# Kernel tuning notes

Hardware: AMD Instinct MI355X
Metric: run time of the kernel (lower is better)

## Reference

```python
import jax, jax.numpy as jnp
import numpy as np

N = 2048; K = 2048; D = 256; D_RESHAPE = 800
HA = 256; DA = 128; HK = 128; HC = 128; HS = 256
S = max(10, int(0.1 * K))  # n_sample = 204
BN_SCALE = 1.0 / float(np.sqrt(1.0 + 1e-5))  # eval BatchNorm1d with running stats (0,1)

def leaky(x):
    return jax.nn.leaky_relu(x, 0.01)

def conv2d(x, w, b):
    y = jax.lax.conv_general_dilated(x, w, (1, 1), 'VALID', dimension_numbers=('NCHW', 'OIHW', 'NCHW'))
    return y + b[None, :, None, None]

def maxpool2(x):
    return jax.lax.reduce_window(x, -jnp.inf, jax.lax.max, (1, 1, 2, 2), (1, 1, 2, 2), 'VALID')

def data_transform(x, c1w, c1b, c2w, c2b, ew, eb):
    h = maxpool2(leaky(conv2d(x, c1w, c1b)))   # [n,20,12,12]
    h = maxpool2(leaky(conv2d(h, c2w, c2b)))   # [n,50,4,4]
    h = h.reshape(-1, D_RESHAPE)
    return leaky(h @ ew.T + eb)                # [n,D]

def skip_block(X, w1, b1, w2, b2, w3, b3):
    # Conv1d kernel_size=1 == per-position linear over channels
    X1 = leaky(X @ w1.T + b1) * BN_SCALE       # [n,HC]
    X2 = leaky(X @ w2.T + b2) * BN_SCALE       # [n,HC]
    X3 = leaky(X @ w3.T + b3) * BN_SCALE       # [n,d]
    feat = jax.nn.softmax(X1 @ X2.T, axis=0)   # torch Softmax(dim=1) on [1,n,n] -> axis 0
    return feat @ X3 + X

def mask_scores(A, w1, b1, w2, b2, w3, b3, w4, b4):
    X1 = leaky(A @ w1.T + b1)                  # [n,HK]
    X2 = jnp.tanh(A @ w2.T + b2)               # [n,HK]
    M = X1.T @ X2                              # [HK,HK]
    A3 = leaky(M @ w3.T + b3)                  # [HK,K]
    s = A3.T @ w4[0] + b4[0]                   # [K]
    return jax.nn.softmax(s)

def attention(X, few, feb, vw, vb, uw, ub, aww, awb, ew, eb):
    H = leaky(X @ few.T + feb)                 # [n,HA]
    AV = jnp.tanh(H @ vw.T + vb)
    AU = leaky(H @ uw.T + ub)
    a = leaky((AV * AU) @ aww.T + awb)         # [n,1]
    A = jax.nn.softmax(a.T, axis=1)            # [1,n]
    M = leaky((A @ H) @ ew.T + eb)             # [1,d]
    return M, A

def euclid(X, Y):
    d2 = jnp.sum(X * X, 1)[:, None] + jnp.sum(Y * Y, 1)[None, :] - 2.0 * (X @ Y.T)
    return jnp.sqrt(jnp.maximum(d2, 0.0))


def setup_inputs() -> dict:
    key = jax.random.key(0)
    ks = iter(jax.random.split(key, 70))
    def rn(shape, scale=0.05):
        return jax.random.normal(next(ks), shape, dtype=jnp.float32) * scale
    d = {}
    d['B'] = jax.random.normal(next(ks), (N, 1, 28, 28), dtype=jnp.float32)
    d['KB'] = jax.random.normal(next(ks), (K, 1, 28, 28), dtype=jnp.float32)
    d['dt_c1_w'] = rn((20, 1, 5, 5)); d['dt_c1_b'] = rn((20,))
    d['dt_c2_w'] = rn((50, 20, 5, 5)); d['dt_c2_b'] = rn((50,))
    d['dt_emb_w'] = rn((D, D_RESHAPE)); d['dt_emb_b'] = rn((D,))
    for nm, dd in (('sk1', D), ('sk2', D), ('sk3', K)):
        d[nm + '_w1'] = rn((HC, dd)); d[nm + '_b1'] = rn((HC,))
        d[nm + '_w2'] = rn((HC, dd)); d[nm + '_b2'] = rn((HC,))
        d[nm + '_w3'] = rn((dd, dd)); d[nm + '_b3'] = rn((dd,))
    d['mk_w1'] = rn((HK, K)); d['mk_b1'] = rn((HK,))
    d['mk_w2'] = rn((HK, K)); d['mk_b2'] = rn((HK,))
    d['mk_w3'] = rn((K, HK)); d['mk_b3'] = rn((K,))
    d['mk_w4'] = rn((1, HK)); d['mk_b4'] = rn((1,))
    d['fuse_w'] = rn((D, D + S)); d['fuse_b'] = rn((D,))
    for nm, din in (('a1', D), ('a2', 2 * D)):
        d[nm + '_fe_w'] = rn((HA, din)); d[nm + '_fe_b'] = rn((HA,))
        d[nm + '_v_w'] = rn((DA, HA)); d[nm + '_v_b'] = rn((DA,))
        d[nm + '_u_w'] = rn((DA, HA)); d[nm + '_u_b'] = rn((DA,))
        d[nm + '_aw_w'] = rn((1, DA)); d[nm + '_aw_b'] = rn((1,))
        d[nm + '_emb_w'] = rn((din, HA)); d[nm + '_emb_b'] = rn((din,))
    d['semb_w'] = rn((HS, 2 * D)); d['semb_b'] = rn((HS,))
    d['cls_w'] = rn((1, HS)); d['cls_b'] = rn((1,))
    return d


def reference(B, KB, dt_c1_w, dt_c1_b, dt_c2_w, dt_c2_b, dt_emb_w, dt_emb_b,
              sk1_w1, sk1_b1, sk1_w2, sk1_b2, sk1_w3, sk1_b3,
              sk2_w1, sk2_b1, sk2_w2, sk2_b2, sk2_w3, sk2_b3,
              sk3_w1, sk3_b1, sk3_w2, sk3_b2, sk3_w3, sk3_b3,
              mk_w1, mk_b1, mk_w2, mk_b2, mk_w3, mk_b3, mk_w4, mk_b4,
              fuse_w, fuse_b,
              a1_fe_w, a1_fe_b, a1_v_w, a1_v_b, a1_u_w, a1_u_b, a1_aw_w, a1_aw_b, a1_emb_w, a1_emb_b,
              a2_fe_w, a2_fe_b, a2_v_w, a2_v_b, a2_u_w, a2_u_b, a2_aw_w, a2_aw_b, a2_emb_w, a2_emb_b,
              semb_w, semb_b, cls_w, cls_b):
    B_dt = data_transform(B, dt_c1_w, dt_c1_b, dt_c2_w, dt_c2_b, dt_emb_w, dt_emb_b)
    KB_dt = data_transform(KB, dt_c1_w, dt_c1_b, dt_c2_w, dt_c2_b, dt_emb_w, dt_emb_b)
    Xs = skip_block(B_dt, sk1_w1, sk1_b1, sk1_w2, sk1_b2, sk1_w3, sk1_b3)
    Ks = skip_block(KB_dt, sk2_w1, sk2_b1, sk2_w2, sk2_b2, sk2_w3, sk2_b3)
    # torch detaches the affinity (.detach().numpy())
    aff = euclid(jax.lax.stop_gradient(Xs), jax.lax.stop_gradient(Ks))  # [N,K]
    aff_s = skip_block(aff, sk3_w1, sk3_b1, sk3_w2, sk3_b2, sk3_w3, sk3_b3)
    scores = mask_scores(aff_s, mk_w1, mk_b1, mk_w2, mk_b2, mk_w3, mk_b3, mk_w4, mk_b4)
    idx = jnp.argsort(-scores)[:S]                       # top-S knowledge columns
    B_bag = jax.nn.softmax(aff_s[:, idx], axis=1)        # [N,S], torch Softmax(dim=2)
    B_fuse = leaky(jnp.concatenate([B_dt, B_bag], axis=1) @ fuse_w.T + fuse_b)  # [N,D]
    M1, _ = attention(B_fuse, a1_fe_w, a1_fe_b, a1_v_w, a1_v_b, a1_u_w, a1_u_b, a1_aw_w, a1_aw_b, a1_emb_w, a1_emb_b)
    X2 = jnp.concatenate([B_fuse, jnp.tile(M1, (B_fuse.shape[0], 1))], axis=1)  # [N,2D]
    bvec, A = attention(X2, a2_fe_w, a2_fe_b, a2_v_w, a2_v_b, a2_u_w, a2_u_b, a2_aw_w, a2_aw_b, a2_emb_w, a2_emb_b)
    bvec = leaky(bvec @ semb_w.T + semb_b)               # [1,HS]
    Y = jnp.clip(jax.nn.sigmoid(bvec @ cls_w.T + cls_b), 1e-5, 1.0 - 1e-5)
    return (Y, A)
```

## Files before the change

kernel.cpp:

```cpp
#include <hip/hip_runtime.h>
#include <math.h>

#define LEAKY(x) ((x) > 0.f ? (x) : 0.01f * (x))
static constexpr float BN_SCALE = 0.9999950000374997f;

typedef unsigned short ushort_t;
typedef float f32x4 __attribute__((ext_vector_type(4)));
typedef short bf16x8 __attribute__((ext_vector_type(8)));

__device__ __forceinline__ ushort_t f2bfu(float f) {
  union { float f; unsigned u; } v; v.f = f;
  unsigned r = v.u + 0x7fffu + ((v.u >> 16) & 1u);
  return (ushort_t)(r >> 16);
}
__device__ __forceinline__ float bfu2f(ushort_t u) {
  union { unsigned u; float f; } v; v.u = ((unsigned)u) << 16;
  return v.f;
}

__device__ __forceinline__ void gload16(const ushort_t* g, ushort_t* lds) {
  __builtin_amdgcn_global_load_lds(
      (const __attribute__((address_space(1))) void*)g,
      (__attribute__((address_space(3))) void*)lds, 16, 0, 0);
}

__global__ void fill_out(float* out, int n) {
  int i = blockIdx.x * 256 + threadIdx.x;
  if (i < n) out[i] = 0.25f;
}

struct CvtArgs {
  const float* src[20];
  ushort_t* dst[20];
  int cum[21];
};
__global__ void to_bf16_flat(CvtArgs a) {
  int total = a.cum[20];
  for (int i = blockIdx.x * 256 + threadIdx.x; i < total; i += gridDim.x * 256) {
    int s = 0;
    while (i >= a.cum[s + 1]) ++s;
    int off = i - a.cum[s];
    a.dst[s][off] = f2bfu(a.src[s][off]);
  }
}

struct BiasPk { const float* a[12]; float* out; };
__global__ void bias_pack(BiasPk p) {
  int b = blockIdx.x, t = threadIdx.x;
  p.out[b * 256 + t] = (t < 128) ? p.a[2 * b][t] : p.a[2 * b + 1][t - 128];
}

__global__ void pad_fuse_bf16(const float* __restrict__ w, ushort_t* __restrict__ wp) {
  int idx = blockIdx.x * 256 + threadIdx.x;
  if (idx >= 256 * 512) return;
  int o = idx >> 9, k = idx & 511;
  wp[idx] = (k < 460) ? f2bfu(w[(size_t)o * 460 + k]) : (ushort_t)0;
}

__global__ void w2_relayout(const float* __restrict__ w2, ushort_t* __restrict__ w2p) {
  int idx = blockIdx.x * 256 + threadIdx.x;
  if (idx >= 64 * 640) return;
  int oc = idx / 640, k = idx - oc * 640;
  int tap = k / 24, ic = k - tap * 24;
  float v = 0.f;
  if (oc < 50 && tap < 25 && ic < 20)
    v = w2[(size_t)(oc * 20 + ic) * 25 + tap];
  w2p[idx] = f2bfu(v);
}

__launch_bounds__(256)
__global__ void conv12_mfma(const float* __restrict__ imgB, const float* __restrict__ imgK,
                            const float* __restrict__ w1, const float* __restrict__ b1,
                            const ushort_t* __restrict__ w2p, const float* __restrict__ b2,
                            ushort_t* __restrict__ out800) {
  __shared__ __align__(16) char smem[41472];
  ushort_t* h1T = (ushort_t*)smem;
  ushort_t* As  = (ushort_t*)(smem + 13824);
  ushort_t* Bs  = (ushort_t*)(smem + 32256);
  float* simg = (float*)(smem + 13824);
  float* sw1  = (float*)(smem + 20992);
  float* b1s  = (float*)(smem + 23040);
  float* Cf   = (float*)smem;

  int tid = threadIdx.x;
  int bx = blockIdx.x;
  const float* imgb = (bx < 1024) ? imgB + (size_t)bx * 2 * 784
                                  : imgK + (size_t)(bx - 1024) * 2 * 784;

  for (int i = tid; i < 1568; i += 256) {
    int im = (i >= 784) ? 1 : 0;
    int r = i - im * 784;
    int row = r / 28, col = r - row * 28;
    int sc = (col + (row >> 1)) & 31;
    simg[im * 896 + row * 32 + sc] = imgb[i];
  }
  for (int i = tid; i < 500; i += 256) sw1[i] = w1[i];
  if (tid < 20) b1s[tid] = b1[tid];
  for (int i = tid; i < 288; i += 256) {
    uint2 z; z.x = 0; z.y = 0;
    *(uint2*)&h1T[i * 24 + 20] = z;
  }
  __syncthreads();

  for (int o = tid; o < 1152; o += 256) {
    int im = (o >= 576) ? 1 : 0;
    int rem = o - im * 576;
    int cg = rem / 144;
    int pos = rem - cg * 144;
    int py = pos / 12, px = pos - py * 12;
    int y0 = py * 2, x0 = px * 2;
    float p[6][6];
    #pragma unroll
    for (int yy = 0; yy < 6; ++yy) {
      int rr = y0 + yy;
      int rbase = im * 896 + rr * 32;
      int rot = rr >> 1;
      #pragma unroll
      for (int xx = 0; xx < 6; ++xx)
        p[yy][xx] = simg[rbase + ((x0 + xx + rot) & 31)];
    }
    #pragma unroll
    for (int cc = 0; cc < 5; ++cc) {
      int c = cg * 5 + cc;
      const float* wc = &sw1[c * 25];
      float bb = b1s[c];
      float t0 = bb, t1 = bb, t2 = bb, t3 = bb;
      #pragma unroll
      for (int ky = 0; ky < 5; ++ky)
        #pragma unroll
        for (int kx = 0; kx < 5; ++kx) {
          float wv = wc[ky * 5 + kx];
          t0 += p[ky][kx] * wv;
          t1 += p[ky][kx + 1] * wv;
          t2 += p[ky + 1][kx] * wv;
          t3 += p[ky + 1][kx + 1] * wv;
        }
      float mx = fmaxf(fmaxf(t0, t1), fmaxf(t2, t3));
      h1T[(im * 144 + pos) * 24 + c] = f2bfu(LEAKY(mx));
    }
  }

  int wave = tid >> 6, lane = tid & 63;
  int wm = (wave >> 1) * 64, wn = (wave & 1) * 32;
  int mrow = lane & 15, kq = lane >> 4;

  int sA_r = tid >> 1;
  int sA_j0 = (tid & 1) * 4;
  int sA_im = sA_r >> 6;
  int sA_op = sA_r & 63;
  int sA_oy = sA_op >> 3, sA_ox = sA_op & 7;
  int sB_r = tid >> 2;
  int sB_j0 = (tid & 3) * 2;

  f32x4 acc[4][2];
  #pragma unroll
  for (int i = 0; i < 4; ++i)
    #pragma unroll
    for (int j = 0; j < 2; ++j)
      #pragma unroll
      for (int r = 0; r < 4; ++r) acc[i][j][r] = 0.f;

  bf16x8 wreg[2];
  #pragma unroll
  for (int i = 0; i < 2; ++i)
    wreg[i] = *(const bf16x8*)&w2p[(size_t)sB_r * 640 + (sB_j0 + i) * 8];

  for (int kb = 0; kb < 10; ++kb) {
    __syncthreads();
    #pragma unroll
    for (int i = 0; i < 2; ++i)
      *(bf16x8*)&Bs[sB_r * 72 + (sB_j0 + i) * 8] = wreg[i];
    #pragma unroll
    for (int i = 0; i < 4; ++i) {
      int j = sA_j0 + i;
      int g = kb * 8 + j;
      int tap = g / 3;
      int part = g - tap * 3;
      bf16x8 v = {0, 0, 0, 0, 0, 0, 0, 0};
      if (tap < 25) {
        int ky = tap / 5, kx = tap - ky * 5;
        int pos = (sA_oy + ky) * 12 + sA_ox + kx;
        v = *(const bf16x8*)&h1T[(sA_im * 144 + pos) * 24 + part * 8];
      }
      *(bf16x8*)&As[sA_r * 72 + j * 8] = v;
    }
    if (kb + 1 < 10) {
      #pragma unroll
      for (int i = 0; i < 2; ++i)
        wreg[i] = *(const bf16x8*)&w2p[(size_t)sB_r * 640 + (kb + 1) * 64 + (sB_j0 + i) * 8];
    }
    __syncthreads();
    #pragma unroll
    for (int ks = 0; ks < 2; ++ks) {
      bf16x8 af[4], bf[2];
      #pragma unroll
      for (int mt = 0; mt < 4; ++mt)
        af[mt] = *(const bf16x8*)&As[(wm + mt * 16 + mrow) * 72 + ks * 32 + kq * 8];
      #pragma unroll
      for (int nt = 0; nt < 2; ++nt)
        bf[nt] = *(const bf16x8*)&Bs[(wn + nt * 16 + mrow) * 72 + ks * 32 + kq * 8];
      #pragma unroll
      for (int mt = 0; mt < 4; ++mt)
        #pragma unroll
        for (int nt = 0; nt < 2; ++nt)
          acc[mt][nt] = __builtin_amdgcn_mfma_f32_16x16x32_bf16(af[mt], bf[nt], acc[mt][nt], 0, 0, 0);
    }
  }
  __syncthreads();
  #pragma unroll
  for (int mt = 0; mt < 4; ++mt)
    #pragma unroll
    for (int nt = 0; nt < 2; ++nt) {
      int n0 = wn + nt * 16 + (lane & 15);
      #pragma unroll
      for (int r = 0; r < 4; ++r)
        Cf[(wm + mt * 16 + kq * 4 + r) * 68 + n0] = acc[mt][nt][r];
    }
  __syncthreads();
  for (int o = tid; o < 1600; o += 256) {
    int im = o / 800, oi = o - im * 800;
    int oc = oi >> 4, p = oi & 15, py = p >> 2, px = p & 3;
    int r0 = im * 64 + py * 16 + px * 2;
    float bb = b2[oc];
    float t0 = LEAKY(Cf[r0 * 68 + oc] + bb);
    float t1 = LEAKY(Cf[(r0 + 1) * 68 + oc] + bb);
    float t2 = LEAKY(Cf[(r0 + 8) * 68 + oc] + bb);
    float t3 = LEAKY(Cf[(r0 + 9) * 68 + oc] + bb);
    out800[(size_t)(bx * 2 + im) * 800 + oi] = f2bfu(fmaxf(fmaxf(t0, t1), fmaxf(t2, t3)));
  }
}

enum { EPI_NONE = 0, EPI_LEAKY = 1, EPI_LEAKY_BN = 2, EPI_TANH = 3, EPI_EUCLID = 4,
       EPI_LEAKY_BN_ROW = 5, EPI_RES = 6 };

template <int EPI>
__launch_bounds__(256)
__global__ void gemm_bf16_nt(const ushort_t* __restrict__ A, const ushort_t* __restrict__ B,
                             const float* __restrict__ bias, float* __restrict__ C32,
                             ushort_t* __restrict__ C16, int M, int N, int Kd,
                             const float* __restrict__ e1, const float* __restrict__ e2) {
  __shared__ __align__(16) ushort_t As[2][128 * 32];
  __shared__ __align__(16) ushort_t Bs[2][128 * 32];
  int tid = threadIdx.x;
  int bm = blockIdx.y * 128, bn = blockIdx.x * 128;
  int wave = tid >> 6, lane = tid & 63;
  int wm = (wave >> 1) * 64, wn = (wave & 1) * 64;
  int mrow = lane & 15, kq = lane >> 4;
  int l0 = tid, l1 = tid + 256;
  const ushort_t* ga0 = A + (size_t)(bm + (l0 >> 2)) * Kd + (l0 & 3) * 8;
  const ushort_t* ga1 = A + (size_t)(bm + (l1 >> 2)) * Kd + (l1 & 3) * 8;
  const ushort_t* gb0 = B + (size_t)(bn + (l0 >> 2)) * Kd + (l0 & 3) * 8;
  const ushort_t* gb1 = B + (size_t)(bn + (l1 >> 2)) * Kd + (l1 & 3) * 8;

  f32x4 acc[4][4];
  #pragma unroll
  for (int i = 0; i < 4; ++i)
    #pragma unroll
    for (int j = 0; j < 4; ++j)
      #pragma unroll
      for (int r = 0; r < 4; ++r) acc[i][j][r] = 0.f;

  gload16(ga0, &As[0][l0 * 8]);
  gload16(ga1, &As[0][l1 * 8]);
  gload16(gb0, &Bs[0][l0 * 8]);
  gload16(gb1, &Bs[0][l1 * 8]);
  int nt = Kd >> 5;
  for (int t = 0; t < nt; ++t) {
    int cur = t & 1;
    __syncthreads();
    if (t + 1 < nt) {
      int ko = (t + 1) * 32;
      gload16(ga0 + ko, &As[cur ^ 1][l0 * 8]);
      gload16(ga1 + ko, &As[cur ^ 1][l1 * 8]);
      gload16(gb0 + ko, &Bs[cur ^ 1][l0 * 8]);
      gload16(gb1 + ko, &Bs[cur ^ 1][l1 * 8]);
    }
    bf16x8 af[4], bf[4];
    #pragma unroll
    for (int mt = 0; mt < 4; ++mt)
      af[mt] = *(const bf16x8*)&As[cur][(wm + mt * 16 + mrow) * 32 + kq * 8];
    #pragma unroll
    for (int nt2 = 0; nt2 < 4; ++nt2)
      bf[nt2] = *(const bf16x8*)&Bs[cur][(wn + nt2 * 16 + mrow) * 32 + kq * 8];
    #pragma unroll
    for (int mt = 0; mt < 4; ++mt)
      #pragma unroll
      for (int nt2 = 0; nt2 < 4; ++nt2)
        acc[mt][nt2] = __builtin_amdgcn_mfma_f32_16x16x32_bf16(af[mt], bf[nt2], acc[mt][nt2], 0, 0, 0);
  }
  #pragma unroll
  for (int mt = 0; mt < 4; ++mt)
    #pragma unroll
    for (int nt2 = 0; nt2 < 4; ++nt2) {
      int n_g = bn + wn + nt2 * 16 + (lane & 15);
      #pragma unroll
      for (int r = 0; r < 4; ++r) {
        int m_g = bm + wm + mt * 16 + kq * 4 + r;
        float v = acc[mt][nt2][r];
        if (EPI == EPI_EUCLID) {
          v = e1[m_g] + e2[n_g] - 2.f * v;
          v = sqrtf(fmaxf(v, 0.f));
        } else if (EPI == EPI_RES) {
          v += bfu2f(((const ushort_t*)e1)[(size_t)m_g * N + n_g]);
        } else {
          if (bias) v += bias[(EPI == EPI_LEAKY_BN_ROW) ? m_g : n_g];
          if (EPI == EPI_LEAKY) v = LEAKY(v);
          else if (EPI == EPI_LEAKY_BN || EPI == EPI_LEAKY_BN_ROW) { v = LEAKY(v); v *= BN_SCALE; }
          else if (EPI == EPI_TANH) v = tanhf(v);
        }
        if (C32) C32[(size_t)m_g * N + n_g] = v;
        if (C16) C16[(size_t)m_g * N + n_g] = f2bfu(v);
      }
    }
}

__launch_bounds__(256)
__global__ void gemm_smat_z(const ushort_t* __restrict__ X12, ushort_t* __restrict__ Smat) {
  int z = blockIdx.z;
  const ushort_t* A = X12 + (size_t)z * 2048 * 256;
  const ushort_t* B = A + 128;
  ushort_t* C = Smat + (size_t)z * 2048 * 2048;
  __shared__ __align__(16) ushort_t As[2][128 * 32];
  __shared__ __align__(16) ushort_t Bs[2][128 * 32];
  int tid = threadIdx.x;
  int bm = blockIdx.y * 128, bn = blockIdx.x * 128;
  int wave = tid >> 6, lane = tid & 63;
  int wm = (wave >> 1) * 64, wn = (wave & 1) * 64;
  int mrow = lane & 15, kq = lane >> 4;
  int l0 = tid, l1 = tid + 256;
  const ushort_t* ga0 = A + (size_t)(bm + (l0 >> 2)) * 256 + (l0 & 3) * 8;
  const ushort_t* ga1 = A + (size_t)(bm + (l1 >> 2)) * 256 + (l1 & 3) * 8;
  const ushort_t* gb0 = B + (size_t)(bn + (l0 >> 2)) * 256 + (l0 & 3) * 8;
  const ushort_t* gb1 = B + (size_t)(bn + (l1 >> 2)) * 256 + (l1 & 3) * 8;

  f32x4 acc[4][4];
  #pragma unroll
  for (int i = 0; i < 4; ++i)
    #pragma unroll
    for (int j = 0; j < 4; ++j)
      #pragma unroll
      for (int r = 0; r < 4; ++r) acc[i][j][r] = 0.f;

  gload16(ga0, &As[0][l0 * 8]);
  gload16(ga1, &As[0][l1 * 8]);
  gload16(gb0, &Bs[0][l0 * 8]);
  gload16(gb1, &Bs[0][l1 * 8]);
  for (int t = 0; t < 4; ++t) {
    int cur = t & 1;
    __syncthreads();
    if (t + 1 < 4) {
// ... 307 lines not shown
  const ushort_t* B = X3T + (size_t)z * 256 * 2048;
  const ushort_t* R = dtb + (size_t)z * 2048 * 256;
  ushort_t* C = XsKs + (size_t)z * 2048 * 256;
  __shared__ __align__(16) ushort_t As[2][64 * 32];
  __shared__ __align__(16) ushort_t Bs[2][64 * 32];
  int tid = threadIdx.x;
  int bm = blockIdx.y * 64, bn = blockIdx.x * 64;
  int wave = tid >> 6, lane = tid & 63;
  int wm = (wave >> 1) * 32, wn = (wave & 1) * 32;
  int mrow = lane & 15, kq = lane >> 4;
  const ushort_t* ga = A + (size_t)(bm + (tid >> 2)) * Kd + (tid & 3) * 8;
  const ushort_t* gb = B + (size_t)(bn + (tid >> 2)) * Kd + (tid & 3) * 8;

  f32x4 acc[2][2];
  #pragma unroll
  for (int i = 0; i < 2; ++i)
    #pragma unroll
    for (int j = 0; j < 2; ++j)
      #pragma unroll
      for (int r = 0; r < 4; ++r) acc[i][j][r] = 0.f;

  gload16(ga, &As[0][tid * 8]);
  gload16(gb, &Bs[0][tid * 8]);
  for (int t = 0; t < 64; ++t) {
    int cur = t & 1;
    __syncthreads();
    if (t + 1 < 64) {
      int ko = (t + 1) * 32;
      gload16(ga + ko, &As[cur ^ 1][tid * 8]);
      gload16(gb + ko, &Bs[cur ^ 1][tid * 8]);
    }
    bf16x8 af[2], bf[2];
    #pragma unroll
    for (int mt = 0; mt < 2; ++mt)
      af[mt] = *(const bf16x8*)&As[cur][(wm + mt * 16 + mrow) * 32 + kq * 8];
    #pragma unroll
    for (int nt2 = 0; nt2 < 2; ++nt2)
      bf[nt2] = *(const bf16x8*)&Bs[cur][(wn + nt2 * 16 + mrow) * 32 + kq * 8];
    #pragma unroll
    for (int mt = 0; mt < 2; ++mt)
      #pragma unroll
      for (int nt2 = 0; nt2 < 2; ++nt2)
        acc[mt][nt2] = __builtin_amdgcn_mfma_f32_16x16x32_bf16(af[mt], bf[nt2], acc[mt][nt2], 0, 0, 0);
  }
  #pragma unroll
  for (int mt = 0; mt < 2; ++mt)
    #pragma unroll
    for (int nt2 = 0; nt2 < 2; ++nt2) {
      int n_g = bn + wn + nt2 * 16 + (lane & 15);
      #pragma unroll
      for (int r = 0; r < 4; ++r) {
        int m_g = bm + wm + mt * 16 + kq * 4 + r;
        float v = acc[mt][nt2][r] + bfu2f(R[(size_t)m_g * N + n_g]);
        C[(size_t)m_g * N + n_g] = f2bfu(v);
      }
    }
}

__global__ void gemm_tn_part(const ushort_t* __restrict__ X, float* __restrict__ part) {
  int tx = threadIdx.x & 15, ty = threadIdx.x >> 4;
  int i = blockIdx.y * 16 + ty, j = blockIdx.x * 16 + tx;
  int ks = blockIdx.z;
  float acc = 0.f;
  for (int k = ks * 128; k < ks * 128 + 128; ++k)
    acc += bfu2f(X[(size_t)k * 256 + i]) * bfu2f(X[(size_t)k * 256 + 128 + j]);
  part[(size_t)ks * 16384 + i * 128 + j] = acc;
}
__global__ void gemm_tn_reduce(const float* __restrict__ part, ushort_t* __restrict__ Mm) {
  int idx = blockIdx.x * 256 + threadIdx.x;
  float s = 0.f;
  #pragma unroll
  for (int ks = 0; ks < 16; ++ks) s += part[(size_t)ks * 16384 + idx];
  Mm[idx] = f2bfu(s);
}

__global__ void smax_partA(const ushort_t* __restrict__ Sb, float* __restrict__ pm,
                           float* __restrict__ pl, int N) {
  int z = blockIdx.z;
  const ushort_t* S = Sb + (size_t)z * 2048 * 2048;
  int t = threadIdx.x;
  int col = blockIdx.x * 64 + (t & 63);
  int g = t >> 6;
  int r0 = blockIdx.y * 128 + g;
  float vals[32];
  #pragma unroll
  for (int i = 0; i < 32; ++i)
    vals[i] = bfu2f(S[(size_t)(r0 + 4 * i) * N + col]);
  float m = -1e30f;
  #pragma unroll
  for (int i = 0; i < 32; ++i) m = fmaxf(m, vals[i]);
  float l = 0.f;
  #pragma unroll
  for (int i = 0; i < 32; ++i) l += expf(vals[i] - m);
  __shared__ float rm[4][64], rl[4][64];
  rm[g][t & 63] = m; rl[g][t & 63] = l;
  __syncthreads();
  if (g == 0) {
    int c = t & 63;
    float M0 = rm[0][c], L0 = rl[0][c];
    #pragma unroll
    for (int j = 1; j < 4; ++j) {
      float Mj = rm[j][c], Lj = rl[j][c];
      float nm = fmaxf(M0, Mj);
      L0 = L0 * expf(M0 - nm) + Lj * expf(Mj - nm);
      M0 = nm;
    }
    pm[((size_t)z * 16 + blockIdx.y) * N + col] = M0;
    pl[((size_t)z * 16 + blockIdx.y) * N + col] = L0;
  }
}
__global__ void smax_partB(const float* __restrict__ pm, const float* __restrict__ pl,
                           float* __restrict__ gm, float* __restrict__ gi, int N) {
  int z = blockIdx.y;
  int col = blockIdx.x * 256 + threadIdx.x;
  float m = -1e30f, l = 0.f;
  for (int b = 0; b < 16; ++b) {
    float bm = pm[((size_t)z * 16 + b) * N + col], bl = pl[((size_t)z * 16 + b) * N + col];
    float nm = fmaxf(m, bm);
    l = l * expf(m - nm) + bl * expf(bm - nm);
    m = nm;
  }
  gm[(size_t)z * N + col] = m;
  gi[(size_t)z * N + col] = 1.f / l;
}
__global__ void smax_partC(ushort_t* __restrict__ Sb, const float* __restrict__ gm,
                           const float* __restrict__ gi, int N) {
  int z = blockIdx.z;
  ushort_t* S = Sb + (size_t)z * 2048 * 2048;
  int t = threadIdx.x;
  int col = blockIdx.x * 64 + (t & 63);
  int g = t >> 6;
  float m = gm[(size_t)z * N + col], inv = gi[(size_t)z * N + col];
  int r0 = blockIdx.y * 128 + g;
  #pragma unroll 8
  for (int i = 0; i < 32; ++i) {
    size_t idx = (size_t)(r0 + 4 * i) * N + col;
    S[idx] = f2bfu(expf(bfu2f(S[idx]) - m) * inv);
  }
}

__global__ void row_norm_bf16(const ushort_t* __restrict__ X, float* __restrict__ out, int Kd) {
  int r = blockIdx.x * 2 + (threadIdx.x >> 5);
  int l = threadIdx.x & 31;
  bf16x8 v = *(const bf16x8*)&X[(size_t)r * Kd + l * 8];
  float s = 0.f;
  #pragma unroll
  for (int j = 0; j < 8; ++j) { float f = bfu2f((ushort_t)v[j]); s += f * f; }
  for (int off = 16; off; off >>= 1) s += __shfl_down(s, off, 32);
  if (l == 0) out[r] = s;
}

__global__ void mask_score(const float* __restrict__ A3, const float* __restrict__ w4,
                           const float* __restrict__ b4, float* __restrict__ s) {
  int k = blockIdx.x * 256 + threadIdx.x;
  float acc = b4[0];
  for (int h = 0; h < 128; ++h) acc += A3[(size_t)h * 2048 + k] * w4[h];
  s[k] = acc;
}

__global__ void topk_rank(const float* __restrict__ s, int* __restrict__ idx, int K, int S) {
  __shared__ float sv[2048];
  int t = threadIdx.x;
  for (int i = t; i < K; i += 256) sv[i] = s[i];
  __syncthreads();
  int j = blockIdx.x * 256 + t;
  if (j >= K) return;
  float sj = sv[j];
  int rank = 0;
  #pragma unroll 8
  for (int i = 0; i < 2048; ++i) {
    float si = sv[i];
    rank += (si > sj) || (si == sj && i < j);
  }
  if (rank < S) idx[rank] = j;
}

__global__ void build_cat(const ushort_t* __restrict__ Bdt, const ushort_t* __restrict__ affs,
                          const int* __restrict__ idx, ushort_t* __restrict__ cat) {
  int r = blockIdx.x, t = threadIdx.x;
  __shared__ float vals[256];
  __shared__ float red[256];
  float v = -1e30f;
  if (t < 204) {
    int ix = idx[t];
    ix = ix < 0 ? 0 : (ix > 2047 ? 2047 : ix);
    v = bfu2f(affs[(size_t)r * 2048 + ix]);
  }
  vals[t] = v;
  red[t] = v;
  __syncthreads();
  for (int off = 128; off; off >>= 1) { if (t < off) red[t] = fmaxf(red[t], red[t + off]); __syncthreads(); }
  float m = red[0];
  __syncthreads();
  float e = (t < 204) ? expf(vals[t] - m) : 0.f;
  red[t] = e;
  __syncthreads();
  for (int off = 128; off; off >>= 1) { if (t < off) red[t] += red[t + off]; __syncthreads(); }
  float inv = 1.f / red[0];
  cat[(size_t)r * 512 + t] = Bdt[(size_t)r * 256 + t];
  cat[(size_t)r * 512 + 256 + t] = (t < 204) ? f2bfu(e * inv) : (ushort_t)0;
}

__global__ void attn_gate(const float* __restrict__ AVU, const float* __restrict__ aww,
                          const float* __restrict__ awb, float* __restrict__ a, int n) {
  int wave = threadIdx.x >> 6, lane = threadIdx.x & 63;
  int r = blockIdx.x * 4 + wave;
  if (r >= n) return;
  float s = 0.f;
  #pragma unroll
  for (int j = 0; j < 2; ++j) {
    int d = lane + 64 * j;
    s += AVU[(size_t)r * 256 + d] * AVU[(size_t)r * 256 + 128 + d] * aww[d];
  }
  for (int off = 32; off; off >>= 1) s += __shfl_down(s, off);
  if (lane == 0) {
    float acc = s + awb[0];
    a[r] = LEAKY(acc);
  }
}

__global__ void softmax_vec(const float* __restrict__ x, float* __restrict__ y,
                            float* __restrict__ y2, int n) {
  __shared__ float red[256];
  int t = threadIdx.x;
  float m = -1e30f;
  for (int i = t; i < n; i += 256) m = fmaxf(m, x[i]);
  red[t] = m;
  __syncthreads();
  for (int off = 128; off; off >>= 1) { if (t < off) red[t] = fmaxf(red[t], red[t + off]); __syncthreads(); }
  m = red[0];
  __syncthreads();
  float s = 0.f;
  for (int i = t; i < n; i += 256) s += expf(x[i] - m);
  red[t] = s;
  __syncthreads();
  for (int off = 128; off; off >>= 1) { if (t < off) red[t] += red[t + off]; __syncthreads(); }
  float inv = 1.f / red[0];
  for (int i = t; i < n; i += 256) {
    float v = expf(x[i] - m) * inv;
    y[i] = v;
    if (y2) y2[i] = v;
  }
}

__global__ void colsum_part(const float* __restrict__ wv, const ushort_t* __restrict__ H,
                            float* __restrict__ part, int n) {
  int bk = blockIdx.x, c = threadIdx.x;
  float s = 0.f;
  for (int r = bk; r < n; r += 16) s += wv[r] * bfu2f(H[(size_t)r * 256 + c]);
  part[bk * 256 + c] = s;
}
__global__ void colsum_fin(const float* __restrict__ part, float* __restrict__ out) {
  int c = threadIdx.x;
  float s = 0.f;
  #pragma unroll
  for (int k = 0; k < 16; ++k) s += part[k * 256 + c];
  out[c] = s;
}

__global__ void gemv_act(const float* __restrict__ x, const float* __restrict__ W,
                         const float* __restrict__ b, float* __restrict__ out,
                         int O, int Kd, int act) {
  int o = blockIdx.x * blockDim.x + threadIdx.x;
  if (o >= O) return;
  float acc = b ? b[o] : 0.f;
  for (int k = 0; k < Kd; ++k) acc += x[k] * W[(size_t)o * Kd + k];
  if (act == 1) acc = LEAKY(acc);
  out[o] = acc;
}

__global__ void build_cat2(const ushort_t* __restrict__ Bf, const float* __restrict__ M1,
                           ushort_t* __restrict__ cat2) {
  int r = blockIdx.x, t = threadIdx.x;
  cat2[(size_t)r * 512 + t] = (t < 256) ? Bf[(size_t)r * 256 + t] : f2bfu(M1[t - 256]);
}

__global__ void final_head(const float* __restrict__ AH2, const float* __restrict__ embw,
                           const float* __restrict__ embb, const float* __restrict__ sembw,
                           const float* __restrict__ sembb, const float* __restrict__ clsw,
                           const float* __restrict__ clsb, float* __restrict__ Yout) {
  __shared__ float bvec[512];
  __shared__ float red[512];
  int t = threadIdx.x;
  float acc = embb[t];
  for (int c = 0; c < 256; ++c) acc += AH2[c] * embw[(size_t)t * 256 + c];
  bvec[t] = LEAKY(acc);
  __syncthreads();
  float p = 0.f;
  if (t < 256) {
    float a2 = sembb[t];
    for (int c = 0; c < 512; ++c) a2 += bvec[c] * sembw[(size_t)t * 512 + c];
    a2 = LEAKY(a2);
    p = a2 * clsw[t];
  }
  red[t] = p;
  __syncthreads();
  for (int off = 256; off; off >>= 1) { if (t < off) red[t] += red[t + off]; __syncthreads(); }
  if (t == 0) {
    float y = red[0] + clsb[0];
    y = 1.f / (1.f + expf(-y));
    y = fminf(fmaxf(y, 1e-5f), 1.f - 1e-5f);
    Yout[0] = y;
  }
}

extern "C" void kernel_launch(void* const* d_in, const int* in_sizes, int n_in,
                              void* d_out, int out_size, void* d_ws, size_t ws_size,
                              hipStream_t stream) {
  auto IN = [&](int i) { return (const float*)d_in[i]; };
  (void)n_in; (void)in_sizes; (void)out_size;

  const int S = 204;
  float* out_f = (float*)d_out;

  float* W = (float*)d_ws;
  size_t off = 0;
  auto F = [&](size_t n) { float* p = W + off; off += n; return p; };
  auto FU = [&](size_t nus) { return (ushort_t*)F((nus + 1) / 2); };

  ushort_t* dt_b  = FU((size_t)4096 * 256);
  ushort_t* XsKs  = FU((size_t)4096 * 256);
  ushort_t* X12b  = FU((size_t)4096 * 256);
  ushort_t* X3sb  = FU((size_t)4096 * 256);
  ushort_t* aff_b = FU((size_t)2048 * 2048);
  float* AVU   = F((size_t)2048 * 256);
  ushort_t* Mm_b = FU((size_t)128 * 128);
  float* svec  = F(2048);
  int*   idxb  = (int*)F(256);
  float* avec  = F(2048);
  float* Awv   = F(2048);
  float* AH    = F(256);
  float* M1v   = F(256);
  float* AH2   = F(256);
  float* nxy   = F(4096);
  float* part  = F(4096);
  float* sm_pm = F((size_t)2 * 16 * 2048);
  float* sm_pl = F((size_t)2 * 16 * 2048);
  float* sm_gm = F(2 * 2048);
  float* sm_gi = F(2 * 2048);
  float* pbias = F(6 * 256);

  size_t wo = 0;
  ushort_t* warena = (ushort_t*)F(3250000);
  auto WA = [&](size_t n) { ushort_t* p = warena + wo; wo = (wo + n + 15) & ~(size_t)15; return p; };
  ushort_t* w2p   = WA(40960);
  ushort_t* embb_ = WA(204800);
  ushort_t* s1w1 = WA(32768); ushort_t* s1w2 = WA(32768); ushort_t* s1w3 = WA(65536);
  ushort_t* s2w1 = WA(32768); ushort_t* s2w2 = WA(32768); ushort_t* s2w3 = WA(65536);
  ushort_t* s3w1 = WA(262144); ushort_t* s3w2 = WA(262144); ushort_t* s3w3 = WA(4194304);
  ushort_t* mw1 = WA(262144); ushort_t* mw2 = WA(262144); ushort_t* mw3 = WA(262144);
  ushort_t* fwp = WA(131072);
  ushort_t* a1fe = WA(65536); ushort_t* a1v = WA(32768); ushort_t* a1u = WA(32768);
  ushort_t* a2fe = WA(131072); ushort_t* a2v = WA(32768); ushort_t* a2u = WA(32768);
  (void)s1w2; (void)s2w2; (void)s3w2; (void)mw2; (void)a1u; (void)a2u;

  float* pool = F((size_t)4194304);

  const size_t NEED_BYTES = off * 4;
  if (ws_size < NEED_BYTES) {
    fill_out<<<9, 256, 0, stream>>>(out_f, 2049);
    return;
  }

  ushort_t* h2h_b   = (ushort_t*)pool;
  ushort_t* SmatB   = (ushort_t*)pool;
  ushort_t* X3b_b   = (ushort_t*)(pool + 2097152);
  float* A3   = pool;
  float* tnpt = pool + 262144;
  ushort_t* cat_b   = (ushort_t*)pool;
  ushort_t* cat2_b  = (ushort_t*)(pool + 524288);
  ushort_t* Bfuse_b = (ushort_t*)(pool + 1048576);
  ushort_t* Hbuf_b  = (ushort_t*)(pool + 1310720);

  CvtArgs ca;
  const float* srcs[20] = { IN(6), IN(8), IN(10), IN(12), IN(14), IN(16), IN(18),
                            IN(20), IN(22), IN(24), IN(26), IN(28), IN(30),
                            IN(36), IN(38), IN(40), IN(46), IN(48), IN(50), IN(4) };
  ushort_t* dsts[20] = { embb_, s1w1, s1w2, s1w3, s2w1, s2w2, s2w3,
                         s3w1, s3w2, s3w3, mw1, mw2, mw3,
                         a1fe, a1v, a1u, a2fe, a2v, a2u, w2p };
  int lens[20] = { 204800, 32768, 32768, 65536, 32768, 32768, 65536,
                   262144, 262144, 4194304, 262144, 262144, 262144,
                   65536, 32768, 32768, 131072, 32768, 32768, 0 };
  int cum = 0;
  for (int i = 0; i < 20; ++i) {
    ca.src[i] = srcs[i]; ca.dst[i] = dsts[i];
    ca.cum[i] = cum; cum += lens[i];
  }
  ca.cum[20] = cum;
  to_bf16_flat<<<2048, 256, 0, stream>>>(ca);
  w2_relayout<<<160, 256, 0, stream>>>(IN(4), w2p);
  pad_fuse_bf16<<<512, 256, 0, stream>>>(IN(34), fwp);
  BiasPk bp;
  const float* bsrc[12] = { IN(9), IN(11), IN(15), IN(17), IN(21), IN(23),
                            IN(27), IN(29), IN(39), IN(41), IN(49), IN(51) };
  for (int i = 0; i < 12; ++i) bp.a[i] = bsrc[i];
  bp.out = pbias;
  bias_pack<<<6, 256, 0, stream>>>(bp);
  float* pb_sk1 = pbias, *pb_sk2 = pbias + 256, *pb_sk3 = pbias + 512;
  float* pb_msk = pbias + 768, *pb_a1 = pbias + 1024, *pb_a2 = pbias + 1280;

  conv12_mfma<<<2048, 256, 0, stream>>>(IN(0), IN(1), IN(2), IN(3), w2p, IN(5), h2h_b);
  gemm_bf16_nt64<EPI_LEAKY><<<dim3(4, 64), 256, 0, stream>>>(
      h2h_b, embb_, IN(7), nullptr, dt_b, 4096, 256, 800);

  gemm_nt64_dual<EPI_LEAKY_BN><<<dim3(4, 64), 256, 0, stream>>>(
      dt_b, s1w1, s2w1, pb_sk1, pb_sk2, X12b, 4096, 256, 256, 2048);
  gemm_w3T_z<<<dim3(32, 4, 2), 256, 0, stream>>>(s1w3, s2w3, IN(13), IN(19), dt_b, X3sb);
  gemm_smat_z<<<dim3(16, 16, 2), 256, 0, stream>>>(X12b, SmatB);
  smax_partA<<<dim3(32, 16, 2), 256, 0, stream>>>(SmatB, sm_pm, sm_pl, 2048);
  smax_partB<<<dim3(8, 2), 256, 0, stream>>>(sm_pm, sm_pl, sm_gm, sm_gi, 2048);
  smax_partC<<<dim3(32, 16, 2), 256, 0, stream>>>(SmatB, sm_gm, sm_gi, 2048);
  gemm_ntt_res64_z<<<dim3(4, 32, 2), 256, 0, stream>>>(SmatB, X3sb, dt_b, XsKs);

  row_norm_bf16<<<2048, 64, 0, stream>>>(XsKs, nxy, 256);
  gemm_bf16_nt<EPI_EUCLID><<<dim3(16, 16), 256, 0, stream>>>(
      XsKs, XsKs + (size_t)2048 * 256, nullptr, nullptr, aff_b, 2048, 2048, 256,
      nxy, nxy + 2048);

  gemm_bf16_nt64<EPI_LEAKY_BN><<<dim3(4, 32), 256, 0, stream>>>(
      aff_b, s3w1, pb_sk3, nullptr, X12b, 2048, 256, 2048);
  gemm_smat_z<<<dim3(16, 16, 1), 256, 0, stream>>>(X12b, SmatB);
  gemm_bf16_nt<EPI_LEAKY_BN_ROW><<<dim3(16, 16), 256, 0, stream>>>(
      s3w3, aff_b, IN(25), nullptr, X3b_b, 2048, 2048, 2048, nullptr, nullptr);
  smax_partA<<<dim3(32, 16, 1), 256, 0, stream>>>(SmatB, sm_pm, sm_pl, 2048);
  smax_partB<<<dim3(8, 1), 256, 0, stream>>>(sm_pm, sm_pl, sm_gm, sm_gi, 2048);
  smax_partC<<<dim3(32, 16, 1), 256, 0, stream>>>(SmatB, sm_gm, sm_gi, 2048);
  gemm_bf16_nt<EPI_RES><<<dim3(16, 16), 256, 0, stream>>>(
      SmatB, X3b_b, nullptr, nullptr, aff_b, 2048, 2048, 2048,
      (const float*)aff_b, nullptr);
  ushort_t* affs_b = aff_b;

  gemm_nt64_split<EPI_LEAKY, EPI_TANH><<<dim3(4, 32), 256, 0, stream>>>(
      affs_b, mw1, pb_msk, nullptr, X12b, 2048, 256, 2048, 128);
  gemm_tn_part<<<dim3(8, 8, 16), 256, 0, stream>>>(X12b, tnpt);
  gemm_tn_reduce<<<64, 256, 0, stream>>>(tnpt, Mm_b);
  gemm_bf16_nt64<EPI_LEAKY><<<dim3(32, 2), 256, 0, stream>>>(
      Mm_b, mw3, IN(31), A3, nullptr, 128, 2048, 128);
  mask_score<<<8, 256, 0, stream>>>(A3, IN(32), IN(33), svec);
  topk_rank<<<8, 256, 0, stream>>>(svec, idxb, 2048, S);

  build_cat<<<2048, 256, 0, stream>>>(dt_b, affs_b, idxb, cat_b);
  gemm_bf16_nt64<EPI_LEAKY><<<dim3(4, 32), 256, 0, stream>>>(
      cat_b, fwp, IN(35), nullptr, Bfuse_b, 2048, 256, 512);

  gemm_bf16_nt64<EPI_LEAKY><<<dim3(4, 32), 256, 0, stream>>>(
      Bfuse_b, a1fe, IN(37), nullptr, Hbuf_b, 2048, 256, 256);
  gemm_nt64_split<EPI_TANH, EPI_LEAKY><<<dim3(4, 32), 256, 0, stream>>>(
      Hbuf_b, a1v, pb_a1, AVU, nullptr, 2048, 256, 256, 128);
  attn_gate<<<512, 256, 0, stream>>>(AVU, IN(42), IN(43), avec, 2048);
  softmax_vec<<<1, 256, 0, stream>>>(avec, Awv, nullptr, 2048);
  colsum_part<<<16, 256, 0, stream>>>(Awv, Hbuf_b, part, 2048);
  colsum_fin<<<1, 256, 0, stream>>>(part, AH);
  gemv_act<<<1, 256, 0, stream>>>(AH, IN(44), IN(45), M1v, 256, 256, 1);
  build_cat2<<<2048, 512, 0, stream>>>(Bfuse_b, M1v, cat2_b);

  gemm_bf16_nt64<EPI_LEAKY><<<dim3(4, 32), 256, 0, stream>>>(
      cat2_b, a2fe, IN(47), nullptr, Hbuf_b, 2048, 256, 512);
  gemm_nt64_split<EPI_TANH, EPI_LEAKY><<<dim3(4, 32), 256, 0, stream>>>(
      Hbuf_b, a2v, pb_a2, AVU, nullptr, 2048, 256, 256, 128);
  attn_gate<<<512, 256, 0, stream>>>(AVU, IN(52), IN(53), avec, 2048);
  softmax_vec<<<1, 256, 0, stream>>>(avec, Awv, out_f + 1, 2048);
  colsum_part<<<16, 256, 0, stream>>>(Awv, Hbuf_b, part, 2048);
  colsum_fin<<<1, 256, 0, stream>>>(part, AH2);

  final_head<<<1, 512, 0, stream>>>(AH2, IN(54), IN(55), IN(56), IN(57),
                                    IN(58), IN(59), out_f);
}
```

Measured before the change: 908.9 us.

## Gather conv2 A-fragments from LDS directly; parallelize gemv, mask score, final head

The conv2 MFMA stage no longer stages an im2col A tile in shared memory. Each wave gathers its A fragments straight from the h1T buffer, which shrinks LDS use and removes one copy pass. The first w2 weight prefetch is hoisted before the conv1 phase. Several small serial kernels (mask_score, gemv_act, final_head) are rewritten to use more blocks or wave-level shuffle reductions with coalesced weight reads, trading extra launch parallelism against small reduction overhead.

After: 925.7 us. Within noise of the previous version (+1.9%).

```diff
diff --git a/kernel.cpp b/kernel.cpp
--- a/kernel.cpp
+++ b/kernel.cpp
@@ -73,13 +73,12 @@
                             const float* __restrict__ w1, const float* __restrict__ b1,
                             const ushort_t* __restrict__ w2p, const float* __restrict__ b2,
                             ushort_t* __restrict__ out800) {
-  __shared__ __align__(16) char smem[41472];
+  __shared__ __align__(16) char smem[34816];
   ushort_t* h1T = (ushort_t*)smem;
-  ushort_t* As  = (ushort_t*)(smem + 13824);
-  ushort_t* Bs  = (ushort_t*)(smem + 32256);
+  ushort_t* Bs  = (ushort_t*)(smem + 13824);
   float* simg = (float*)(smem + 13824);
   float* sw1  = (float*)(smem + 20992);
-  float* b1s  = (float*)(smem + 23040);
+  float* b1s  = (float*)(smem + 22992);
   float* Cf   = (float*)smem;
 
   int tid = threadIdx.x;
@@ -100,6 +99,14 @@
     uint2 z; z.x = 0; z.y = 0;
     *(uint2*)&h1T[i * 24 + 20] = z;
   }
+
+  int sB_r = tid >> 2;
+  int sB_j0 = (tid & 3) * 2;
+  bf16x8 wreg[2];
+  #pragma unroll
+  for (int i = 0; i < 2; ++i)
+    wreg[i] = *(const bf16x8*)&w2p[(size_t)sB_r * 640 + (sB_j0 + i) * 8];
+
   __syncthreads();
 
   for (int o = tid; o < 1152; o += 256) {
@@ -144,13 +151,15 @@
   int wm = (wave >> 1) * 64, wn = (wave & 1) * 32;
   int mrow = lane & 15, kq = lane >> 4;
 
-  int sA_r = tid >> 1;
-  int sA_j0 = (tid & 1) * 4;
-  int sA_im = sA_r >> 6;
-  int sA_op = sA_r & 63;
-  int sA_oy = sA_op >> 3, sA_ox = sA_op & 7;
-  int sB_r = tid >> 2;
-  int sB_j0 = (tid & 3) * 2;
+  int imv[4], oyv[4], oxv[4];
+  #pragma unroll
+  for (int mt = 0; mt < 4; ++mt) {
+    int r = wm + mt * 16 + mrow;
+    imv[mt] = r >> 6;
+    int op = r & 63;
+    oyv[mt] = op >> 3;
+    oxv[mt] = op & 7;
+  }
 
   f32x4 acc[4][2];
   #pragma unroll
@@ -159,43 +168,31 @@
     for (int j = 0; j < 2; ++j)
       #pragma unroll
       for (int r = 0; r < 4; ++r) acc[i][j][r] = 0.f;
-
-  bf16x8 wreg[2];
-  #pragma unroll
-  for (int i = 0; i < 2; ++i)
-    wreg[i] = *(const bf16x8*)&w2p[(size_t)sB_r * 640 + (sB_j0 + i) * 8];
 
   for (int kb = 0; kb < 10; ++kb) {
     __syncthreads();
     #pragma unroll
     for (int i = 0; i < 2; ++i)
       *(bf16x8*)&Bs[sB_r * 72 + (sB_j0 + i) * 8] = wreg[i];
-    #pragma unroll
-    for (int i = 0; i < 4; ++i) {
-      int j = sA_j0 + i;
-      int g = kb * 8 + j;
+    if (kb + 1 < 10) {
+      #pragma unroll
+      for (int i = 0; i < 2; ++i)
+        wreg[i] = *(const bf16x8*)&w2p[(size_t)sB_r * 640 + (kb + 1) * 64 + (sB_j0 + i) * 8];
+    }
+    __syncthreads();
+    #pragma unroll
+    for (int ks = 0; ks < 2; ++ks) {
+      int g = kb * 8 + ks * 4 + kq;
       int tap = g / 3;
       int part = g - tap * 3;
-      bf16x8 v = {0, 0, 0, 0, 0, 0, 0, 0};
-      if (tap < 25) {
-        int ky = tap / 5, kx = tap - ky * 5;
-        int pos = (sA_oy + ky) * 12 + sA_ox + kx;
-        v = *(const bf16x8*)&h1T[(sA_im * 144 + pos) * 24 + part * 8];
+      int tc = tap < 25 ? tap : 24;
+      int ky = tc / 5, kx = tc - ky * 5;
+      bf16x8 af[4], bf[2];
+      #pragma unroll
+      for (int mt = 0; mt < 4; ++mt) {
+        int pos = (oyv[mt] + ky) * 12 + oxv[mt] + kx;
+        af[mt] = *(const bf16x8*)&h1T[(imv[mt] * 144 + pos) * 24 + part * 8];
       }
-      *(bf16x8*)&As[sA_r * 72 + j * 8] = v;
-    }
-    if (kb + 1 < 10) {
-      #pragma unroll
-      for (int i = 0; i < 2; ++i)
-        wreg[i] = *(const bf16x8*)&w2p[(size_t)sB_r * 640 + (kb + 1) * 64 + (sB_j0 + i) * 8];
-    }
-    __syncthreads();
-    #pragma unroll
-    for (int ks = 0; ks < 2; ++ks) {
-      bf16x8 af[4], bf[2];
-      #pragma unroll
-      for (int mt = 0; mt < 4; ++mt)
-        af[mt] = *(const bf16x8*)&As[(wm + mt * 16 + mrow) * 72 + ks * 32 + kq * 8];
       #pragma unroll
       for (int nt = 0; nt < 2; ++nt)
         bf[nt] = *(const bf16x8*)&Bs[(wn + nt * 16 + mrow) * 72 + ks * 32 + kq * 8];
@@ -809,10 +806,17 @@
 
 __global__ void mask_score(const float* __restrict__ A3, const float* __restrict__ w4,
                            const float* __restrict__ b4, float* __restrict__ s) {
-  int k = blockIdx.x * 256 + threadIdx.x;
-  float acc = b4[0];
-  for (int h = 0; h < 128; ++h) acc += A3[(size_t)h * 2048 + k] * w4[h];
-  s[k] = acc;
+  __shared__ float red[4][64];
+  int t = threadIdx.x;
+  int col = blockIdx.x * 64 + (t & 63);
+  int seg = t >> 6;
+  float acc = 0.f;
+  for (int h = seg * 32; h < seg * 32 + 32; ++h)
+    acc += A3[(size_t)h * 2048 + col] * w4[h];
+  red[seg][t & 63] = acc;
+  __syncthreads();
+  if (seg == 0)
+    s[col] = red[0][t] + red[1][t] + red[2][t] + red[3][t] + b4[0];
 }
 
 __global__ void topk_rank(const float* __restrict__ s, int* __restrict__ idx, int K, int S) {
@@ -918,12 +922,16 @@
 __global__ void gemv_act(const float* __restrict__ x, const float* __restrict__ W,
                          const float* __restrict__ b, float* __restrict__ out,
                          int O, int Kd, int act) {
-  int o = blockIdx.x * blockDim.x + threadIdx.x;
+  int wave = threadIdx.x >> 6, lane = threadIdx.x & 63;
+  int o = blockIdx.x * 4 + wave;
   if (o >= O) return;
-  float acc = b ? b[o] : 0.f;
-  for (int k = 0; k < Kd; ++k) acc += x[k] * W[(size_t)o * Kd + k];
-  if (act == 1) acc = LEAKY(acc);
-  out[o] = acc;
+  float s = 0.f;
+  for (int c = lane; c < Kd; c += 64) s += x[c] * W[(size_t)o * Kd + c];
+  for (int off = 32; off; off >>= 1) s += __shfl_down(s, off);
+  if (lane == 0) {
+    float acc = s + (b ? b[o] : 0.f);
+    out[o] = act ? LEAKY(acc) : acc;
+  }
 }
 
 __global__ void build_cat2(const ushort_t* __restrict__ Bf, const float* __restrict__ M1,
@@ -936,28 +944,49 @@
                            const float* __restrict__ embb, const float* __restrict__ sembw,
                            const float* __restrict__ sembb, const float* __restrict__ clsw,
                            const float* __restrict__ clsb, float* __restrict__ Yout) {
+  __shared__ float sAH[256];
   __shared__ float bvec[512];
-  __shared__ float red[512];
+  __shared__ float prod[256];
   int t = threadIdx.x;
-  float acc = embb[t];
-  for (int c = 0; c < 256; ++c) acc += AH2[c] * embw[(size_t)t * 256 + c];
-  bvec[t] = LEAKY(acc);
-  __syncthreads();
-  float p = 0.f;
-  if (t < 256) {
-    float a2 = sembb[t];
-    for (int c = 0; c < 512; ++c) a2 += bvec[c] * sembw[(size_t)t * 512 + c];
-    a2 = LEAKY(a2);
-    p = a2 * clsw[t];
-  }
-  red[t] = p;
-  __syncthreads();
-  for (int off = 256; off; off >>= 1) { if (t < off) red[t] += red[t + off]; __syncthreads(); }
-  if (t == 0) {
-    float y = red[0] + clsb[0];
-    y = 1.f / (1.f + expf(-y));
-    y = fminf(fmaxf(y, 1e-5f), 1.f - 1e-5f);
-    Yout[0] = y;
+  int wave = t >> 6, lane = t & 63;
+  if (t < 256) sAH[t] = AH2[t];
+  __syncthreads();
+  for (int i = 0; i < 64; ++i) {
+    int o = wave * 64 + i;
+    float s = 0.f;
+    #pragma unroll
+    for (int j = 0; j < 4; ++j) {
+      int c = lane + 64 * j;
+      s += sAH[c] * embw[(size_t)o * 256 + c];
+    }
+    for (int off = 32; off; off >>= 1) s += __shfl_down(s, off);
+    if (lane == 0) bvec[o] = LEAKY(s + embb[o]);
+  }
+  __syncthreads();
+  for (int i = 0; i < 32; ++i) {
+    int o = wave * 32 + i;
+    float s = 0.f;
+    #pragma unroll
+    for (int j = 0; j < 8; ++j) {
+      int c = lane + 64 * j;
+      s += bvec[c] * sembw[(size_t)o * 512 + c];
+    }
+    for (int off = 32; off; off >>= 1) s += __shfl_down(s, off);
+    if (lane == 0) {
+      float a2 = LEAKY(s + sembb[o]);
+      prod[o] = a2 * clsw[o];
+    }
+  }
+  __syncthreads();
+  if (t < 64) {
+    float s = prod[t] + prod[t + 64] + prod[t + 128] + prod[t + 192];
+    for (int off = 32; off; off >>= 1) s += __shfl_down(s, off);
+    if (t == 0) {
+      float y = s + clsb[0];
+      y = 1.f / (1.f + expf(-y));
+      y = fminf(fmaxf(y, 1e-5f), 1.f - 1e-5f);
+      Yout[0] = y;
+    }
   }
 }
 
@@ -1094,7 +1123,7 @@
   gemm_tn_reduce<<<64, 256, 0, stream>>>(tnpt, Mm_b);
   gemm_bf16_nt64<EPI_LEAKY><<<dim3(32, 2), 256, 0, stream>>>(
       Mm_b, mw3, IN(31), A3, nullptr, 128, 2048, 128);
-  mask_score<<<8, 256, 0, stream>>>(A3, IN(32), IN(33), svec);
+  mask_score<<<32, 256, 0, stream>>>(A3, IN(32), IN(33), svec);
   topk_rank<<<8, 256, 0, stream>>>(svec, idxb, 2048, S);
 
   build_cat<<<2048, 256, 0, stream>>>(dt_b, affs_b, idxb, cat_b);
@@ -1109,7 +1138,7 @@
   softmax_vec<<<1, 256, 0, stream>>>(avec, Awv, nullptr, 2048);
   colsum_part<<<16, 256, 0, stream>>>(Awv, Hbuf_b, part, 2048);
   colsum_fin<<<1, 256, 0, stream>>>(part, AH);
-  gemv_act<<<1, 256, 0, stream>>>(AH, IN(44), IN(45), M1v, 256, 256, 1);
+  gemv_act<<<64, 256, 0, stream>>>(AH, IN(44), IN(45), M1v, 256, 256, 1);
   build_cat2<<<2048, 512, 0, stream>>>(Bfuse_b, M1v, cat2_b);
 
   gemm_bf16_nt64<EPI_LEAKY><<<dim3(4, 32), 256, 0, stream>>>(
```
